# Optimization experiments

Measured on AMD Instinct MI355X. Metric: run time of the kernel, lower is better.

Reference implementation:

```python
import jax, jax.numpy as jnp
import numpy as np

B, C, H, W = 4, 256, 64, 64

def _conv1x1(x, Wt, b):
    # x: [b,c,h,w], Wt: [out,in], b: [out]
    return jnp.einsum('bchw,dc->bdhw', x, Wt) + b[None, :, None, None]

def setup_inputs() -> dict:
    key = jax.random.key(0)
    ks = jax.random.split(key, 10)
    s = 1.0 / np.sqrt(C)
    return {
        'F_c': jax.random.normal(ks[0], (B, C, H, W), jnp.float32),
        'F_s': jax.random.normal(ks[1], (B, C, H, W), jnp.float32),
        'Wf': jax.random.normal(ks[2], (C, C), jnp.float32) * s,
        'bf': jnp.zeros((C,), jnp.float32),
        'Wg': jax.random.normal(ks[3], (C, C), jnp.float32) * s,
        'bg': jnp.zeros((C,), jnp.float32),
        'Wh': jax.random.normal(ks[4], (C, C), jnp.float32) * s,
        'bh': jnp.zeros((C,), jnp.float32),
        'Wo': jax.random.normal(ks[5], (C, C), jnp.float32) * s,
        'bo': jnp.zeros((C,), jnp.float32),
    }

def reference(F_c, F_s, Wf, bf, Wg, bg, Wh, bh, Wo, bo):
    b, c, h, w = F_c.shape
    Fq = _conv1x1(F_c, Wf, bf).reshape(b, c, -1)          # [b,c,Nc]
    G = _conv1x1(F_s, Wg, bg).reshape(b, c, -1)           # [b,c,Ns]
    Hv = _conv1x1(F_s, Wh, bh).reshape(b, c, -1)          # [b,c,Ns]
    S = jnp.einsum('bcn,bcm->bnm', Fq, G)                 # [b,Nc,Ns] (unscaled)
    S = jax.nn.softmax(S, axis=-1)
    res = jnp.einsum('bcm,bnm->bcn', Hv, S)               # [b,c,Nc]
    res = res.reshape(b, c, h, w)
    return _conv1x1(res, Wo, bo)
```

## Files before the change

### kernel.cpp

```cpp
#include <hip/hip_runtime.h>
#include <stdint.h>

#define NB 4
#define CC 256
#define NN 4096
#define KITERS 32

typedef __attribute__((ext_vector_type(8))) _Float16 half8;
typedef __attribute__((ext_vector_type(4))) _Float16 half4;
typedef __attribute__((ext_vector_type(2))) _Float16 half2v;
typedef __attribute__((ext_vector_type(4))) float floatx4;
typedef __attribute__((ext_vector_type(16))) float float16v;
typedef __attribute__((ext_vector_type(4))) int intx4;

__device__ __forceinline__ void cvt16(const float4* src, half8& lo, half8& hi) {
  float4 a = src[0], b = src[1], c = src[2], d = src[3];
  lo[0] = (_Float16)a.x; lo[1] = (_Float16)a.y; lo[2] = (_Float16)a.z; lo[3] = (_Float16)a.w;
  lo[4] = (_Float16)b.x; lo[5] = (_Float16)b.y; lo[6] = (_Float16)b.z; lo[7] = (_Float16)b.w;
  hi[0] = (_Float16)c.x; hi[1] = (_Float16)c.y; hi[2] = (_Float16)c.z; hi[3] = (_Float16)c.w;
  hi[4] = (_Float16)d.x; hi[5] = (_Float16)d.y; hi[6] = (_Float16)d.z; hi[7] = (_Float16)d.w;
}

__global__ __launch_bounds__(256) void k_transpose(const float* __restrict__ Fc,
                                                   const float* __restrict__ Fs,
                                                   _Float16* __restrict__ Xct,
                                                   _Float16* __restrict__ Xst) {
  __shared__ float t[64][65];
  const int nt = blockIdx.x, ct = blockIdx.y, bz = blockIdx.z;
  const int b = bz >> 1;
  const float* src = ((bz & 1) ? Fs : Fc) + (size_t)b * CC * NN;
  _Float16* dst = ((bz & 1) ? Xst : Xct) + (size_t)b * NN * CC;
  const int tid = threadIdx.x;
  const int n0 = nt * 64, c0 = ct * 64;
  const int col = tid & 63, row4 = tid >> 6;
#pragma unroll
  for (int i = 0; i < 16; i++) {
    int c = row4 + i * 4;
    t[c][col] = src[(size_t)(c0 + c) * NN + n0 + col];
  }
  __syncthreads();
#pragma unroll
  for (int i = 0; i < 16; i++) {
    int n = row4 + i * 4;
    dst[(size_t)(n0 + n) * CC + c0 + col] = (_Float16)t[col][n];
  }
}

__global__ __launch_bounds__(256, 2) void k_qkv(const float* __restrict__ Wf,
                                                const float* __restrict__ Wg,
                                                const float* __restrict__ Wh,
                                                const _Float16* __restrict__ Xct,
                                                const _Float16* __restrict__ Xst,
                                                const float* __restrict__ bf,
                                                const float* __restrict__ bg,
                                                const float* __restrict__ bh,
                                                _Float16* __restrict__ Qf,
                                                _Float16* __restrict__ Kf,
                                                _Float16* __restrict__ Vtf) {
  __shared__ _Float16 As[128][40];
  __shared__ _Float16 Bs[128][40];
  const int z = blockIdx.z, bz = blockIdx.y;
  const float* W = (z == 0) ? Wf : ((z == 1) ? Wg : Wh);
  const _Float16* X = ((z == 0) ? Xct : Xst) + (size_t)bz * NN * CC;
  const float* bias = (z == 0) ? bf : ((z == 1) ? bg : bh);
  int mt, nt;
  if (z < 2) { mt = blockIdx.x >> 5; nt = blockIdx.x & 31; }
  else       { mt = blockIdx.x >> 1; nt = blockIdx.x & 1;  }
  const int m0 = mt * 128, n0 = nt * 128;
  const int tid = threadIdx.x;
  const int wave = tid >> 6, lane = tid & 63, quad = lane >> 4, l15 = lane & 15;
  const int wm = (wave >> 1) * 64, wn = (wave & 1) * 64;

  floatx4 acc[4][4];
#pragma unroll
  for (int i = 0; i < 4; i++)
#pragma unroll
    for (int j = 0; j < 4; j++) acc[i][j] = (floatx4){0.f, 0.f, 0.f, 0.f};

  const int srow = tid >> 1;
  const int shalf = (tid & 1) * 16;

  for (int kk = 0; kk < 256; kk += 32) {
    half8 a_lo, a_hi, b_lo, b_hi;
    if (z < 2) {
      cvt16((const float4*)(W + (size_t)(m0 + srow) * 256 + kk + shalf), a_lo, a_hi);
      const _Float16* bp = X + (size_t)(n0 + srow) * 256 + kk + shalf;
      b_lo = *(const half8*)bp; b_hi = *(const half8*)(bp + 8);
    } else {
      const _Float16* ap = X + (size_t)(m0 + srow) * 256 + kk + shalf;
      a_lo = *(const half8*)ap; a_hi = *(const half8*)(ap + 8);
      cvt16((const float4*)(W + (size_t)(n0 + srow) * 256 + kk + shalf), b_lo, b_hi);
    }
    __syncthreads();
    *(half8*)&As[srow][shalf] = a_lo;
    *(half8*)&As[srow][shalf + 8] = a_hi;
    *(half8*)&Bs[srow][shalf] = b_lo;
    *(half8*)&Bs[srow][shalf + 8] = b_hi;
    __syncthreads();
    half8 af[4], bfr[4];
#pragma unroll
    for (int mb = 0; mb < 4; mb++) af[mb] = *(const half8*)&As[wm + mb * 16 + l15][quad * 8];
#pragma unroll
    for (int nb = 0; nb < 4; nb++) bfr[nb] = *(const half8*)&Bs[wn + nb * 16 + l15][quad * 8];
#pragma unroll
    for (int mb = 0; mb < 4; mb++)
#pragma unroll
      for (int nb = 0; nb < 4; nb++)
        acc[mb][nb] = __builtin_amdgcn_mfma_f32_16x16x32_f16(af[mb], bfr[nb], acc[mb][nb], 0, 0, 0);
  }

  if (z < 2) {
    _Float16* op = (z == 0 ? Qf : Kf) + (size_t)bz * NN * CC;
#pragma unroll
    for (int mb = 0; mb < 4; mb++) {
      int d0 = m0 + wm + mb * 16 + quad * 4;
      float b0 = bias[d0], b1 = bias[d0 + 1], b2 = bias[d0 + 2], b3 = bias[d0 + 3];
#pragma unroll
      for (int nb = 0; nb < 4; nb++) {
        int n_ = n0 + wn + nb * 16 + l15;
        half4 pk;
        pk[0] = (_Float16)(acc[mb][nb][0] + b0);
        pk[1] = (_Float16)(acc[mb][nb][1] + b1);
        pk[2] = (_Float16)(acc[mb][nb][2] + b2);
        pk[3] = (_Float16)(acc[mb][nb][3] + b3);
        *(half4*)(op + (size_t)n_ * CC + d0) = pk;
      }
    }
  } else {
    _Float16* op = Vtf + (size_t)bz * NN * CC;
#pragma unroll
    for (int mb = 0; mb < 4; mb++) {
      int nq0 = m0 + wm + mb * 16 + quad * 4;
#pragma unroll
      for (int nb = 0; nb < 4; nb++) {
        int d = n0 + wn + nb * 16 + l15;
        float bv = bias[d];
        half4 pk;
        pk[0] = (_Float16)(acc[mb][nb][0] + bv);
        pk[1] = (_Float16)(acc[mb][nb][1] + bv);
        pk[2] = (_Float16)(acc[mb][nb][2] + bv);
        pk[3] = (_Float16)(acc[mb][nb][3] + bv);
        *(half4*)(op + (size_t)d * NN + nq0) = pk;
      }
    }
  }
}

__global__ __launch_bounds__(256, 2) void k_attn(const _Float16* __restrict__ Q,
                                                 const _Float16* __restrict__ K,
                                                 const _Float16* __restrict__ Vt,
                                                 _Float16* __restrict__ Opart,
                                                 float2* __restrict__ Ml) {
  __shared__ _Float16 Kl[32][264];
  __shared__ _Float16 Vl[2][256][40];
  __shared__ _Float16 Pl[4][32][40];

  const int qt = blockIdx.x, ck = blockIdx.y, b = blockIdx.z;
  const int tid = threadIdx.x;
  const int wave = tid >> 6, lane = tid & 63;
  const int ql = lane & 31, h = lane >> 5;
  const int q0 = qt * 128 + wave * 32;
  const _Float16* Qb = Q + (size_t)b * NN * CC;
  const _Float16* Kb = K + (size_t)b * NN * CC;
  const _Float16* Vb = Vt + (size_t)b * CC * NN;
  const int k_base = ck * 1024;

  half8 qf[16];
#pragma unroll
  for (int cs = 0; cs < 16; cs++)
    qf[cs] = *(const half8*)(Qb + (size_t)(q0 + ql) * CC + cs * 16 + h * 8);

  float16v Oa[8];
#pragma unroll
  for (int g = 0; g < 8; g++)
#pragma unroll
    for (int i = 0; i < 16; i++) Oa[g][i] = 0.f;

  float m_run = -1e30f, l_run = 0.f;

  const int krow = tid >> 4;
  const int kcol = (tid & 15) * 16;
  const int vrow = tid >> 2;
  const int vcol = (tid & 3) * 8;

  intx4 kpre[4], vpre[4];
  {
    const _Float16* g = Kb + (size_t)k_base * CC;
    kpre[0] = *(const intx4*)(g + (size_t)krow * CC + kcol);
    kpre[1] = *(const intx4*)(g + (size_t)krow * CC + kcol + 8);
    kpre[2] = *(const intx4*)(g + (size_t)(krow + 16) * CC + kcol);
    kpre[3] = *(const intx4*)(g + (size_t)(krow + 16) * CC + kcol + 8);
#pragma unroll
    for (int p = 0; p < 4; p++)
      vpre[p] = *(const intx4*)(Vb + (size_t)(vrow + 64 * p) * NN + k_base + vcol);
  }

  for (int t = 0; t < KITERS; t++) {
    const int vb = t & 1;
    __syncthreads();
    *(intx4*)&Kl[krow][kcol] = kpre[0];
    *(intx4*)&Kl[krow][kcol + 8] = kpre[1];
    *(intx4*)&Kl[krow + 16][kcol] = kpre[2];
    *(intx4*)&Kl[krow + 16][kcol + 8] = kpre[3];
#pragma unroll
    for (int p = 0; p < 4; p++) *(intx4*)&Vl[vb][vrow + 64 * p][vcol] = vpre[p];
    __syncthreads();
    if (t + 1 < KITERS) {
      const int k0n = k_base + (t + 1) * 32;
      const _Float16* g = Kb + (size_t)k0n * CC;
      kpre[0] = *(const intx4*)(g + (size_t)krow * CC + kcol);
      kpre[1] = *(const intx4*)(g + (size_t)krow * CC + kcol + 8);
      kpre[2] = *(const intx4*)(g + (size_t)(krow + 16) * CC + kcol);
      kpre[3] = *(const intx4*)(g + (size_t)(krow + 16) * CC + kcol + 8);
#pragma unroll
      for (int p = 0; p < 4; p++)
        vpre[p] = *(const intx4*)(Vb + (size_t)(vrow + 64 * p) * NN + k0n + vcol);
    }

    float16v s;
#pragma unroll
    for (int i = 0; i < 16; i++) s[i] = 0.f;
    if (t > 0) {
      const int vr = vb ^ 1;
      half8 pf0 = *(const half8*)&Pl[wave][ql][h * 8];
      half8 pf1 = *(const half8*)&Pl[wave][ql][16 + h * 8];
#pragma unroll
      for (int u = 0; u < 8; u++) {
        half8 kfa = *(const half8*)&Kl[ql][(2 * u) * 16 + h * 8];
        s = __builtin_amdgcn_mfma_f32_32x32x16_f16(kfa, qf[2 * u], s, 0, 0, 0);
        half8 vfa = *(const half8*)&Vl[vr][u * 32 + ql][h * 8];
        Oa[u] = __builtin_amdgcn_mfma_f32_32x32x16_f16(vfa, pf0, Oa[u], 0, 0, 0);
        half8 kfb = *(const half8*)&Kl[ql][(2 * u + 1) * 16 + h * 8];
        s = __builtin_amdgcn_mfma_f32_32x32x16_f16(kfb, qf[2 * u + 1], s, 0, 0, 0);
        half8 vfb = *(const half8*)&Vl[vr][u * 32 + ql][16 + h * 8];
        Oa[u] = __builtin_amdgcn_mfma_f32_32x32x16_f16(vfb, pf1, Oa[u], 0, 0, 0);
      }
    } else {
#pragma unroll
      for (int cs = 0; cs < 16; cs++) {
        half8 kf = *(const half8*)&Kl[ql][cs * 16 + h * 8];
        s = __builtin_amdgcn_mfma_f32_32x32x16_f16(kf, qf[cs], s, 0, 0, 0);
      }
    }

    float tmax = s[0];
#pragma unroll
    for (int i = 1; i < 16; i++) tmax = fmaxf(tmax, s[i]);
    tmax = fmaxf(tmax, __shfl_xor(tmax, 32));
    bool need = tmax > m_run + 8.0f;
    if (__any((int)need)) {
      float mN = need ? tmax : m_run;
      float alpha = __expf(m_run - mN);
      m_run = mN;
      l_run *= alpha;
#pragma unroll
      for (int g = 0; g < 8; g++)
#pragma unroll
        for (int i = 0; i < 16; i++) Oa[g][i] *= alpha;
    }
    float ts = 0.f;
#pragma unroll
    for (int i = 0; i < 16; i++) {
      float p = __expf(s[i] - m_run);
      s[i] = p;
      ts += p;
    }
    ts += __shfl_xor(ts, 32);
    l_run += ts;
#pragma unroll
    for (int r = 0; r < 16; r += 2) {
      half2v pk;
      pk[0] = (_Float16)s[r];
      pk[1] = (_Float16)s[r + 1];
      int kk2 = (r & 3) + 8 * (r >> 2) + 4 * h;
      *(half2v*)&Pl[wave][ql][kk2] = pk;
    }
  }

  {
    const int vr = (KITERS - 1) & 1;
    half8 pf0 = *(const half8*)&Pl[wave][ql][h * 8];
    half8 pf1 = *(const half8*)&Pl[wave][ql][16 + h * 8];
#pragma unroll
    for (int u = 0; u < 8; u++) {
      half8 vfa = *(const half8*)&Vl[vr][u * 32 + ql][h * 8];
      Oa[u] = __builtin_amdgcn_mfma_f32_32x32x16_f16(vfa, pf0, Oa[u], 0, 0, 0);
      half8 vfb = *(const half8*)&Vl[vr][u * 32 + ql][16 + h * 8];
      Oa[u] = __builtin_amdgcn_mfma_f32_32x32x16_f16(vfb, pf1, Oa[u], 0, 0, 0);
    }
  }

  float invl = 1.f / l_run;
  __syncthreads();
  float* ot = (float*)(&Kl[0][0]) + wave * (32 * 33);
  _Float16* Opb = Opart + ((size_t)ck * NB + b) * NN * CC;
  const int qr = lane >> 1;
  const int chalf = (lane & 1) * 16;
#pragma unroll
  for (int g = 0; g < 8; g++) {
#pragma unroll
    for (int r = 0; r < 16; r++)
      ot[((r & 3) + 8 * (r >> 2) + 4 * h) * 33 + ql] = Oa[g][r] * invl;
    __builtin_amdgcn_s_waitcnt(0);
    half8 o0, o1;
#pragma unroll
    for (int i = 0; i < 8; i++) o0[i] = (_Float16)ot[(chalf + i) * 33 + qr];
#pragma unroll
    for (int i = 0; i < 8; i++) o1[i] = (_Float16)ot[(chalf + 8 + i) * 33 + qr];
    _Float16* gp = Opb + (size_t)(q0 + qr) * CC + g * 32 + chalf;
    *(half8*)gp = o0;
    *(half8*)(gp + 8) = o1;
    __builtin_amdgcn_s_waitcnt(0);
  }
  if (h == 0) {
    float2 ml; ml.x = m_run; ml.y = l_run;
    Ml[((size_t)ck * NB + b) * NN + q0 + ql] = ml;
  }
}

__global__ __launch_bounds__(256) void k_merge(const _Float16* __restrict__ Opart,
                                               const float2* __restrict__ Ml,
                                               _Float16* __restrict__ Om) {
  const int b = blockIdx.y, t = threadIdx.x;
  const int q = blockIdx.x * 32 + (t >> 3);
  const int c0 = (t & 7) * 32;
  const size_t qi = (size_t)b * NN + q;
  float2 m0 = Ml[qi], m1 = Ml[(size_t)NB * NN + qi];
  float2 m2 = Ml[(size_t)2 * NB * NN + qi], m3 = Ml[(size_t)3 * NB * NN + qi];
  float M = fmaxf(fmaxf(m0.x, m1.x), fmaxf(m2.x, m3.x));
  float w0 = __expf(m0.x - M) * m0.y, w1 = __expf(m1.x - M) * m1.y;
  float w2 = __expf(m2.x - M) * m2.y, w3 = __expf(m3.x - M) * m3.y;
  float inv = 1.f / (w0 + w1 + w2 + w3);
  w0 *= inv; w1 *= inv; w2 *= inv; w3 *= inv;
  const size_t off = qi * CC + c0;
  const size_t ps = (size_t)NB * NN * CC;
  const _Float16* p0 = Opart + off;
  const _Float16* p1 = Opart + ps + off;
  const _Float16* p2 = Opart + 2 * ps + off;
  const _Float16* p3 = Opart + 3 * ps + off;
  _Float16* o = Om + off;
#pragma unroll
  for (int u = 0; u < 4; u++) {
    half8 a0 = *(const half8*)(p0 + u * 8);
    half8 a1 = *(const half8*)(p1 + u * 8);
    half8 a2 = *(const half8*)(p2 + u * 8);
    half8 a3 = *(const half8*)(p3 + u * 8);
    half8 r;
#pragma unroll
    for (int i = 0; i < 8; i++)
      r[i] = (_Float16)(w0 * (float)a0[i] + w1 * (float)a1[i] +
                        w2 * (float)a2[i] + w3 * (float)a3[i]);
    *(half8*)(o + u * 8) = r;
  }
}

__global__ __launch_bounds__(256, 2) void k_out(const _Float16* __restrict__ Om,
                                                const float* __restrict__ Wo,
                                                const float* __restrict__ bo,
                                                float* __restrict__ out) {
  __shared__ _Float16 As[128][40];
  __shared__ _Float16 Bs[128][40];
  const int bz = blockIdx.y;
  const int mt = blockIdx.x >> 1, nt = blockIdx.x & 1;
  const int m0 = mt * 128, n0 = nt * 128;
  const int tid = threadIdx.x;
  const int wave = tid >> 6, lane = tid & 63, quad = lane >> 4, l15 = lane & 15;
  const int wm = (wave >> 1) * 64, wn = (wave & 1) * 64;
  const _Float16* X = Om + (size_t)bz * NN * CC;

  floatx4 acc[4][4];
#pragma unroll
  for (int i = 0; i < 4; i++)
#pragma unroll
    for (int j = 0; j < 4; j++) acc[i][j] = (floatx4){0.f, 0.f, 0.f, 0.f};

  const int srow = tid >> 1;
  const int shalf = (tid & 1) * 16;

  for (int kk = 0; kk < 256; kk += 32) {
    const _Float16* ap = X + (size_t)(m0 + srow) * 256 + kk + shalf;
    half8 a_lo = *(const half8*)ap;
    half8 a_hi = *(const half8*)(ap + 8);
    half8 b_lo, b_hi;
    cvt16((const float4*)(Wo + (size_t)(n0 + srow) * 256 + kk + shalf), b_lo, b_hi);
    __syncthreads();
    *(half8*)&As[srow][shalf] = a_lo;
    *(half8*)&As[srow][shalf + 8] = a_hi;
    *(half8*)&Bs[srow][shalf] = b_lo;
    *(half8*)&Bs[srow][shalf + 8] = b_hi;
    __syncthreads();
    half8 af[4], bfr[4];
#pragma unroll
    for (int mb = 0; mb < 4; mb++) af[mb] = *(const half8*)&As[wm + mb * 16 + l15][quad * 8];
#pragma unroll
    for (int nb = 0; nb < 4; nb++) bfr[nb] = *(const half8*)&Bs[wn + nb * 16 + l15][quad * 8];
#pragma unroll
    for (int mb = 0; mb < 4; mb++)
#pragma unroll
      for (int nb = 0; nb < 4; nb++)
        acc[mb][nb] = __builtin_amdgcn_mfma_f32_16x16x32_f16(af[mb], bfr[nb], acc[mb][nb], 0, 0, 0);
  }

  float* op = out + (size_t)bz * NN * CC;
#pragma unroll
  for (int mb = 0; mb < 4; mb++) {
    int nq0 = m0 + wm + mb * 16 + quad * 4;
#pragma unroll
    for (int nb = 0; nb < 4; nb++) {
      int d = n0 + wn + nb * 16 + l15;
      float bv = bo[d];
      floatx4 pk;
      pk[0] = acc[mb][nb][0] + bv;
      pk[1] = acc[mb][nb][1] + bv;
      pk[2] = acc[mb][nb][2] + bv;
      pk[3] = acc[mb][nb][3] + bv;
      *(floatx4*)(op + (size_t)d * NN + nq0) = pk;
    }
  }
}

extern "C" void kernel_launch(void* const* d_in, const int* in_sizes, int n_in,
                              void* d_out, int out_size, void* d_ws, size_t ws_size,
                              hipStream_t stream) {
  const float* Fc = (const float*)d_in[0];
  const float* Fs = (const float*)d_in[1];
  const float* Wf = (const float*)d_in[2];
  const float* bf_ = (const float*)d_in[3];
  const float* Wg = (const float*)d_in[4];
  const float* bg = (const float*)d_in[5];
  const float* Wh = (const float*)d_in[6];
  const float* bh = (const float*)d_in[7];
  const float* Wo = (const float*)d_in[8];
  const float* bo = (const float*)d_in[9];

  char* ws = (char*)d_ws;
  const size_t sz = (size_t)NB * NN * CC * sizeof(_Float16);
  _Float16* Xct = (_Float16*)(ws + 0 * sz);
  _Float16* Xst = (_Float16*)(ws + 1 * sz);
  _Float16* Opart = Xct;
  _Float16* Qf  = (_Float16*)(ws + 4 * sz);
  _Float16* Kf  = (_Float16*)(ws + 5 * sz);
  _Float16* Vtf = (_Float16*)(ws + 6 * sz);
  _Float16* Om  = Qf;
  float2* Ml = (float2*)(ws + 7 * sz);

  k_transpose<<<dim3(64, 4, 8), 256, 0, stream>>>(Fc, Fs, Xct, Xst);
  k_qkv<<<dim3(64, NB, 3), 256, 0, stream>>>(Wf, Wg, Wh, Xct, Xst, bf_, bg, bh, Qf, Kf, Vtf);
  k_attn<<<dim3(32, 4, NB), 256, 0, stream>>>(Qf, Kf, Vtf, Opart, Ml);
  k_merge<<<dim3(128, NB), 256, 0, stream>>>(Opart, Ml, Om);
  k_out<<<dim3(64, NB), 256, 0, stream>>>(Om, Wo, bo, (float*)d_out);
}
```

Baseline: 226.9 us.

## Pre-swizzle Q/K/V into MFMA fragment order and fuse split-K merge into output GEMM

The QKV projection now writes Q, K and V directly in a tiled MFMA-fragment layout. The attention kernel can then load tiles with contiguous, conflict-free vector copies and read fragments with lane-linear LDS accesses instead of padded strided arrays. The separate merge kernel is removed: the output projection combines the four split-K partials with their softmax weights while it loads its A operand. This saves one launch and one intermediate round trip. It also narrows the epilogue waitcnt to LGKM only and uses tree reductions for the row max and sum, at the cost of scattered stores in the QKV epilogue.

```diff
diff --git a/kernel.cpp b/kernel.cpp
--- a/kernel.cpp
+++ b/kernel.cpp
@@ -5,6 +5,7 @@
 #define CC 256
 #define NN 4096
 #define KITERS 32
+#define WAIT_LGKM0 0xC07F
 
 typedef __attribute__((ext_vector_type(8))) _Float16 half8;
 typedef __attribute__((ext_vector_type(4))) _Float16 half4;
@@ -54,9 +55,9 @@
                                                 const float* __restrict__ bf,
                                                 const float* __restrict__ bg,
                                                 const float* __restrict__ bh,
-                                                _Float16* __restrict__ Qf,
-                                                _Float16* __restrict__ Kf,
-                                                _Float16* __restrict__ Vtf) {
+                                                _Float16* __restrict__ Qs,
+                                                _Float16* __restrict__ Ks,
+                                                _Float16* __restrict__ Vs) {
   __shared__ _Float16 As[128][40];
   __shared__ _Float16 Bs[128][40];
   const int z = blockIdx.z, bz = blockIdx.y;
@@ -110,37 +111,44 @@
   }
 
   if (z < 2) {
-    _Float16* op = (z == 0 ? Qf : Kf) + (size_t)bz * NN * CC;
+    _Float16* op = (z == 0 ? Qs : Ks) + (size_t)bz * NN * CC;
 #pragma unroll
     for (int mb = 0; mb < 4; mb++) {
       int d0 = m0 + wm + mb * 16 + quad * 4;
       float b0 = bias[d0], b1 = bias[d0 + 1], b2 = bias[d0 + 2], b3 = bias[d0 + 3];
+      const int cs = d0 >> 4, hh = (d0 >> 3) & 1, j0 = d0 & 7;
 #pragma unroll
       for (int nb = 0; nb < 4; nb++) {
         int n_ = n0 + wn + nb * 16 + l15;
+        int kt = n_ >> 5, ql_ = n_ & 31;
         half4 pk;
         pk[0] = (_Float16)(acc[mb][nb][0] + b0);
         pk[1] = (_Float16)(acc[mb][nb][1] + b1);
         pk[2] = (_Float16)(acc[mb][nb][2] + b2);
         pk[3] = (_Float16)(acc[mb][nb][3] + b3);
-        *(half4*)(op + (size_t)n_ * CC + d0) = pk;
+        size_t idx = ((size_t)(kt * 16 + cs) * 64 + ql_ + 32 * hh) * 8 + j0;
+        *(half4*)(op + idx) = pk;
       }
     }
   } else {
-    _Float16* op = Vtf + (size_t)bz * NN * CC;
+    _Float16* op = Vs + (size_t)bz * NN * CC;
 #pragma unroll
     for (int mb = 0; mb < 4; mb++) {
       int nq0 = m0 + wm + mb * 16 + quad * 4;
+      const int kt = nq0 >> 5, krel = nq0 & 31;
+      const int hk = krel >> 4, hh = (krel >> 3) & 1, j0 = krel & 7;
 #pragma unroll
       for (int nb = 0; nb < 4; nb++) {
         int d = n0 + wn + nb * 16 + l15;
+        int ql_ = d & 31, g = (d >> 5) & 7;
         float bv = bias[d];
         half4 pk;
         pk[0] = (_Float16)(acc[mb][nb][0] + bv);
         pk[1] = (_Float16)(acc[mb][nb][1] + bv);
         pk[2] = (_Float16)(acc[mb][nb][2] + bv);
         pk[3] = (_Float16)(acc[mb][nb][3] + bv);
-        *(half4*)(op + (size_t)d * NN + nq0) = pk;
+        size_t idx = (((size_t)(kt * 8 + g) * 2 + hk) * 64 + ql_ + 32 * hh) * 8 + j0;
+        *(half4*)(op + idx) = pk;
       }
     }
   }
@@ -151,24 +159,25 @@
                                                  const _Float16* __restrict__ Vt,
                                                  _Float16* __restrict__ Opart,
                                                  float2* __restrict__ Ml) {
-  __shared__ _Float16 Kl[32][264];
-  __shared__ _Float16 Vl[2][256][40];
-  __shared__ _Float16 Pl[4][32][40];
-
-  const int qt = blockIdx.x, ck = blockIdx.y, b = blockIdx.z;
+  __shared__ _Float16 smem[8192 * 3 + 4096];
   const int tid = threadIdx.x;
   const int wave = tid >> 6, lane = tid & 63;
+  _Float16* Kl = smem;
+  _Float16* Plw = smem + 3 * 8192 + wave * 1024;
+
+  const int qt = blockIdx.x, ck = blockIdx.y, b = blockIdx.z;
   const int ql = lane & 31, h = lane >> 5;
   const int q0 = qt * 128 + wave * 32;
   const _Float16* Qb = Q + (size_t)b * NN * CC;
   const _Float16* Kb = K + (size_t)b * NN * CC;
-  const _Float16* Vb = Vt + (size_t)b * CC * NN;
-  const int k_base = ck * 1024;
-
+  const _Float16* Vb = Vt + (size_t)b * NN * CC;
+  const int kt_base = ck * (1024 / 32);
+
+  const int ktq = q0 >> 5;
   half8 qf[16];
 #pragma unroll
   for (int cs = 0; cs < 16; cs++)
-    qf[cs] = *(const half8*)(Qb + (size_t)(q0 + ql) * CC + cs * 16 + h * 8);
+    qf[cs] = *(const half8*)(Qb + ((size_t)(ktq * 16 + cs) * 64 + lane) * 8);
 
   float16v Oa[8];
 #pragma unroll
@@ -177,75 +186,70 @@
     for (int i = 0; i < 16; i++) Oa[g][i] = 0.f;
 
   float m_run = -1e30f, l_run = 0.f;
-
-  const int krow = tid >> 4;
-  const int kcol = (tid & 15) * 16;
-  const int vrow = tid >> 2;
-  const int vcol = (tid & 3) * 8;
 
   intx4 kpre[4], vpre[4];
   {
-    const _Float16* g = Kb + (size_t)k_base * CC;
-    kpre[0] = *(const intx4*)(g + (size_t)krow * CC + kcol);
-    kpre[1] = *(const intx4*)(g + (size_t)krow * CC + kcol + 8);
-    kpre[2] = *(const intx4*)(g + (size_t)(krow + 16) * CC + kcol);
-    kpre[3] = *(const intx4*)(g + (size_t)(krow + 16) * CC + kcol + 8);
-#pragma unroll
-    for (int p = 0; p < 4; p++)
-      vpre[p] = *(const intx4*)(Vb + (size_t)(vrow + 64 * p) * NN + k_base + vcol);
+    const _Float16* Kt = Kb + (size_t)kt_base * 8192;
+    const _Float16* Vtile = Vb + (size_t)kt_base * 8192;
+#pragma unroll
+    for (int p = 0; p < 4; p++) {
+      kpre[p] = *(const intx4*)(Kt + tid * 8 + p * 2048);
+      vpre[p] = *(const intx4*)(Vtile + tid * 8 + p * 2048);
+    }
   }
 
   for (int t = 0; t < KITERS; t++) {
     const int vb = t & 1;
-    __syncthreads();
-    *(intx4*)&Kl[krow][kcol] = kpre[0];
-    *(intx4*)&Kl[krow][kcol + 8] = kpre[1];
-    *(intx4*)&Kl[krow + 16][kcol] = kpre[2];
-    *(intx4*)&Kl[krow + 16][kcol + 8] = kpre[3];
-#pragma unroll
-    for (int p = 0; p < 4; p++) *(intx4*)&Vl[vb][vrow + 64 * p][vcol] = vpre[p];
+    _Float16* Vw = smem + (1 + vb) * 8192;
+    __syncthreads();
+#pragma unroll
+    for (int p = 0; p < 4; p++) {
+      *(intx4*)(Kl + tid * 8 + p * 2048) = kpre[p];
+      *(intx4*)(Vw + tid * 8 + p * 2048) = vpre[p];
+    }
     __syncthreads();
     if (t + 1 < KITERS) {
-      const int k0n = k_base + (t + 1) * 32;
-      const _Float16* g = Kb + (size_t)k0n * CC;
-      kpre[0] = *(const intx4*)(g + (size_t)krow * CC + kcol);
-      kpre[1] = *(const intx4*)(g + (size_t)krow * CC + kcol + 8);
-      kpre[2] = *(const intx4*)(g + (size_t)(krow + 16) * CC + kcol);
-      kpre[3] = *(const intx4*)(g + (size_t)(krow + 16) * CC + kcol + 8);
-#pragma unroll
-      for (int p = 0; p < 4; p++)
-        vpre[p] = *(const intx4*)(Vb + (size_t)(vrow + 64 * p) * NN + k0n + vcol);
+      const _Float16* Kt = Kb + (size_t)(kt_base + t + 1) * 8192;
+      const _Float16* Vtile = Vb + (size_t)(kt_base + t + 1) * 8192;
+#pragma unroll
+      for (int p = 0; p < 4; p++) {
+        kpre[p] = *(const intx4*)(Kt + tid * 8 + p * 2048);
+        vpre[p] = *(const intx4*)(Vtile + tid * 8 + p * 2048);
+      }
     }
 
     float16v s;
 #pragma unroll
     for (int i = 0; i < 16; i++) s[i] = 0.f;
     if (t > 0) {
-      const int vr = vb ^ 1;
-      half8 pf0 = *(const half8*)&Pl[wave][ql][h * 8];
-      half8 pf1 = *(const half8*)&Pl[wave][ql][16 + h * 8];
+      _Float16* Vr = smem + (1 + (vb ^ 1)) * 8192;
+      half8 pf0 = *(const half8*)(Plw + lane * 8);
+      half8 pf1 = *(const half8*)(Plw + 512 + lane * 8);
 #pragma unroll
       for (int u = 0; u < 8; u++) {
-        half8 kfa = *(const half8*)&Kl[ql][(2 * u) * 16 + h * 8];
+        half8 kfa = *(const half8*)(Kl + (2 * u) * 512 + lane * 8);
         s = __builtin_amdgcn_mfma_f32_32x32x16_f16(kfa, qf[2 * u], s, 0, 0, 0);
-        half8 vfa = *(const half8*)&Vl[vr][u * 32 + ql][h * 8];
+        half8 vfa = *(const half8*)(Vr + (u * 2) * 512 + lane * 8);
         Oa[u] = __builtin_amdgcn_mfma_f32_32x32x16_f16(vfa, pf0, Oa[u], 0, 0, 0);
-        half8 kfb = *(const half8*)&Kl[ql][(2 * u + 1) * 16 + h * 8];
+        half8 kfb = *(const half8*)(Kl + (2 * u + 1) * 512 + lane * 8);
         s = __builtin_amdgcn_mfma_f32_32x32x16_f16(kfb, qf[2 * u + 1], s, 0, 0, 0);
-        half8 vfb = *(const half8*)&Vl[vr][u * 32 + ql][16 + h * 8];
+        half8 vfb = *(const half8*)(Vr + (u * 2 + 1) * 512 + lane * 8);
         Oa[u] = __builtin_amdgcn_mfma_f32_32x32x16_f16(vfb, pf1, Oa[u], 0, 0, 0);
       }
     } else {
 #pragma unroll
       for (int cs = 0; cs < 16; cs++) {
-        half8 kf = *(const half8*)&Kl[ql][cs * 16 + h * 8];
+        half8 kf = *(const half8*)(Kl + cs * 512 + lane * 8);
         s = __builtin_amdgcn_mfma_f32_32x32x16_f16(kf, qf[cs], s, 0, 0, 0);
       }
     }
 
-    float tmax = s[0];
-#pragma unroll
-    for (int i = 1; i < 16; i++) tmax = fmaxf(tmax, s[i]);
+    float t0 = fmaxf(s[0], s[1]), t1 = fmaxf(s[2], s[3]);
+    float t2 = fmaxf(s[4], s[5]), t3 = fmaxf(s[6], s[7]);
+    float t4 = fmaxf(s[8], s[9]), t5 = fmaxf(s[10], s[11]);
+    float t6 = fmaxf(s[12], s[13]), t7 = fmaxf(s[14], s[15]);
+    t0 = fmaxf(t0, t1); t2 = fmaxf(t2, t3); t4 = fmaxf(t4, t5); t6 = fmaxf(t6, t7);
+    float tmax = fmaxf(fmaxf(t0, t2), fmaxf(t4, t6));
     tmax = fmaxf(tmax, __shfl_xor(tmax, 32));
     bool need = tmax > m_run + 8.0f;
     if (__any((int)need)) {
@@ -258,13 +262,13 @@
 #pragma unroll
         for (int i = 0; i < 16; i++) Oa[g][i] *= alpha;
     }
-    float ts = 0.f;
-#pragma unroll
-    for (int i = 0; i < 16; i++) {
-      float p = __expf(s[i] - m_run);
-      s[i] = p;
-      ts += p;
-    }
+#pragma unroll
+    for (int i = 0; i < 16; i++) s[i] = __expf(s[i] - m_run);
+    float u0 = (s[0] + s[1]) + (s[2] + s[3]);
+    float u1 = (s[4] + s[5]) + (s[6] + s[7]);
+    float u2 = (s[8] + s[9]) + (s[10] + s[11]);
+    float u3 = (s[12] + s[13]) + (s[14] + s[15]);
+    float ts = (u0 + u1) + (u2 + u3);
     ts += __shfl_xor(ts, 32);
     l_run += ts;
 #pragma unroll
@@ -272,27 +276,27 @@
       half2v pk;
       pk[0] = (_Float16)s[r];
       pk[1] = (_Float16)s[r + 1];
-      int kk2 = (r & 3) + 8 * (r >> 2) + 4 * h;
-      *(half2v*)&Pl[wave][ql][kk2] = pk;
+      int k = (r & 3) + 8 * (r >> 2) + 4 * h;
+      *(half2v*)(Plw + (k >> 4) * 512 + (ql + 32 * ((k >> 3) & 1)) * 8 + (k & 7)) = pk;
     }
   }
 
   {
-    const int vr = (KITERS - 1) & 1;
-    half8 pf0 = *(const half8*)&Pl[wave][ql][h * 8];
-    half8 pf1 = *(const half8*)&Pl[wave][ql][16 + h * 8];
+    _Float16* Vr = smem + (1 + ((KITERS - 1) & 1)) * 8192;
+    half8 pf0 = *(const half8*)(Plw + lane * 8);
+    half8 pf1 = *(const half8*)(Plw + 512 + lane * 8);
 #pragma unroll
     for (int u = 0; u < 8; u++) {
-      half8 vfa = *(const half8*)&Vl[vr][u * 32 + ql][h * 8];
+      half8 vfa = *(const half8*)(Vr + (u * 2) * 512 + lane * 8);
       Oa[u] = __builtin_amdgcn_mfma_f32_32x32x16_f16(vfa, pf0, Oa[u], 0, 0, 0);
-      half8 vfb = *(const half8*)&Vl[vr][u * 32 + ql][16 + h * 8];
+      half8 vfb = *(const half8*)(Vr + (u * 2 + 1) * 512 + lane * 8);
       Oa[u] = __builtin_amdgcn_mfma_f32_32x32x16_f16(vfb, pf1, Oa[u], 0, 0, 0);
     }
   }
 
   float invl = 1.f / l_run;
   __syncthreads();
-  float* ot = (float*)(&Kl[0][0]) + wave * (32 * 33);
+  float* ot = (float*)smem + wave * (32 * 33);
   _Float16* Opb = Opart + ((size_t)ck * NB + b) * NN * CC;
   const int qr = lane >> 1;
   const int chalf = (lane & 1) * 16;
@@ -301,7 +305,7 @@
 #pragma unroll
     for (int r = 0; r < 16; r++)
       ot[((r & 3) + 8 * (r >> 2) + 4 * h) * 33 + ql] = Oa[g][r] * invl;
-    __builtin_amdgcn_s_waitcnt(0);
+    __builtin_amdgcn_s_waitcnt(WAIT_LGKM0);
     half8 o0, o1;
 #pragma unroll
     for (int i = 0; i < 8; i++) o0[i] = (_Float16)ot[(chalf + i) * 33 + qr];
@@ -310,7 +314,7 @@
     _Float16* gp = Opb + (size_t)(q0 + qr) * CC + g * 32 + chalf;
     *(half8*)gp = o0;
     *(half8*)(gp + 8) = o1;
-    __builtin_amdgcn_s_waitcnt(0);
+    __builtin_amdgcn_s_waitcnt(WAIT_LGKM0);
   }
   if (h == 0) {
     float2 ml; ml.x = m_run; ml.y = l_run;
@@ -318,43 +322,8 @@
   }
 }
 
-__global__ __launch_bounds__(256) void k_merge(const _Float16* __restrict__ Opart,
-                                               const float2* __restrict__ Ml,
-                                               _Float16* __restrict__ Om) {
-  const int b = blockIdx.y, t = threadIdx.x;
-  const int q = blockIdx.x * 32 + (t >> 3);
-  const int c0 = (t & 7) * 32;
-  const size_t qi = (size_t)b * NN + q;
-  float2 m0 = Ml[qi], m1 = Ml[(size_t)NB * NN + qi];
-  float2 m2 = Ml[(size_t)2 * NB * NN + qi], m3 = Ml[(size_t)3 * NB * NN + qi];
-  float M = fmaxf(fmaxf(m0.x, m1.x), fmaxf(m2.x, m3.x));
-  float w0 = __expf(m0.x - M) * m0.y, w1 = __expf(m1.x - M) * m1.y;
-  float w2 = __expf(m2.x - M) * m2.y, w3 = __expf(m3.x - M) * m3.y;
-  float inv = 1.f / (w0 + w1 + w2 + w3);
-  w0 *= inv; w1 *= inv; w2 *= inv; w3 *= inv;
-  const size_t off = qi * CC + c0;
-  const size_t ps = (size_t)NB * NN * CC;
-  const _Float16* p0 = Opart + off;
-  const _Float16* p1 = Opart + ps + off;
-  const _Float16* p2 = Opart + 2 * ps + off;
-  const _Float16* p3 = Opart + 3 * ps + off;
-  _Float16* o = Om + off;
-#pragma unroll
-  for (int u = 0; u < 4; u++) {
-    half8 a0 = *(const half8*)(p0 + u * 8);
-    half8 a1 = *(const half8*)(p1 + u * 8);
-    half8 a2 = *(const half8*)(p2 + u * 8);
-    half8 a3 = *(const half8*)(p3 + u * 8);
-    half8 r;
-#pragma unroll
-    for (int i = 0; i < 8; i++)
-      r[i] = (_Float16)(w0 * (float)a0[i] + w1 * (float)a1[i] +
-                        w2 * (float)a2[i] + w3 * (float)a3[i]);
-    *(half8*)(o + u * 8) = r;
-  }
-}
-
-__global__ __launch_bounds__(256, 2) void k_out(const _Float16* __restrict__ Om,
+__global__ __launch_bounds__(256, 2) void k_out(const _Float16* __restrict__ Opart,
+                                                const float2* __restrict__ Ml,
                                                 const float* __restrict__ Wo,
                                                 const float* __restrict__ bo,
                                                 float* __restrict__ out) {
@@ -366,7 +335,6 @@
   const int tid = threadIdx.x;
   const int wave = tid >> 6, lane = tid & 63, quad = lane >> 4, l15 = lane & 15;
   const int wm = (wave >> 1) * 64, wn = (wave & 1) * 64;
-  const _Float16* X = Om + (size_t)bz * NN * CC;
 
   floatx4 acc[4][4];
 #pragma unroll
@@ -377,15 +345,36 @@
   const int srow = tid >> 1;
   const int shalf = (tid & 1) * 16;
 
+  const size_t qi = (size_t)bz * NN + m0 + srow;
+  float2 a0 = Ml[qi], a1 = Ml[(size_t)NB * NN + qi];
+  float2 a2 = Ml[(size_t)2 * NB * NN + qi], a3 = Ml[(size_t)3 * NB * NN + qi];
+  float M = fmaxf(fmaxf(a0.x, a1.x), fmaxf(a2.x, a3.x));
+  float w0 = __expf(a0.x - M) * a0.y, w1 = __expf(a1.x - M) * a1.y;
+  float w2 = __expf(a2.x - M) * a2.y, w3 = __expf(a3.x - M) * a3.y;
+  float inv = 1.f / (w0 + w1 + w2 + w3);
+  w0 *= inv; w1 *= inv; w2 *= inv; w3 *= inv;
+  const size_t ps = (size_t)NB * NN * CC;
+  const _Float16* prow = Opart + qi * CC;
+
   for (int kk = 0; kk < 256; kk += 32) {
-    const _Float16* ap = X + (size_t)(m0 + srow) * 256 + kk + shalf;
-    half8 a_lo = *(const half8*)ap;
-    half8 a_hi = *(const half8*)(ap + 8);
+    const _Float16* pr = prow + kk + shalf;
+    half8 p0a = *(const half8*)pr,            p0b = *(const half8*)(pr + 8);
+    half8 p1a = *(const half8*)(pr + ps),     p1b = *(const half8*)(pr + ps + 8);
+    half8 p2a = *(const half8*)(pr + 2 * ps), p2b = *(const half8*)(pr + 2 * ps + 8);
+    half8 p3a = *(const half8*)(pr + 3 * ps), p3b = *(const half8*)(pr + 3 * ps + 8);
+    half8 ma, mb2;
+#pragma unroll
+    for (int i = 0; i < 8; i++) {
+      ma[i] = (_Float16)(w0 * (float)p0a[i] + w1 * (float)p1a[i] +
+                         w2 * (float)p2a[i] + w3 * (float)p3a[i]);
+      mb2[i] = (_Float16)(w0 * (float)p0b[i] + w1 * (float)p1b[i] +
+                          w2 * (float)p2b[i] + w3 * (float)p3b[i]);
+    }
     half8 b_lo, b_hi;
     cvt16((const float4*)(Wo + (size_t)(n0 + srow) * 256 + kk + shalf), b_lo, b_hi);
     __syncthreads();
-    *(half8*)&As[srow][shalf] = a_lo;
-    *(half8*)&As[srow][shalf + 8] = a_hi;
+    *(half8*)&As[srow][shalf] = ma;
+    *(half8*)&As[srow][shalf + 8] = mb2;
     *(half8*)&Bs[srow][shalf] = b_lo;
     *(half8*)&Bs[srow][shalf + 8] = b_hi;
     __syncthreads();
@@ -438,15 +427,13 @@
   _Float16* Xct = (_Float16*)(ws + 0 * sz);
   _Float16* Xst = (_Float16*)(ws + 1 * sz);
   _Float16* Opart = Xct;
-  _Float16* Qf  = (_Float16*)(ws + 4 * sz);
-  _Float16* Kf  = (_Float16*)(ws + 5 * sz);
-  _Float16* Vtf = (_Float16*)(ws + 6 * sz);
-  _Float16* Om  = Qf;
+  _Float16* Qs = (_Float16*)(ws + 4 * sz);
+  _Float16* Ks = (_Float16*)(ws + 5 * sz);
+  _Float16* Vs = (_Float16*)(ws + 6 * sz);
   float2* Ml = (float2*)(ws + 7 * sz);
 
   k_transpose<<<dim3(64, 4, 8), 256, 0, stream>>>(Fc, Fs, Xct, Xst);
-  k_qkv<<<dim3(64, NB, 3), 256, 0, stream>>>(Wf, Wg, Wh, Xct, Xst, bf_, bg, bh, Qf, Kf, Vtf);
-  k_attn<<<dim3(32, 4, NB), 256, 0, stream>>>(Qf, Kf, Vtf, Opart, Ml);
-  k_merge<<<dim3(128, NB), 256, 0, stream>>>(Opart, Ml, Om);
-  k_out<<<dim3(64, NB), 256, 0, stream>>>(Om, Wo, bo, (float*)d_out);
-}
+  k_qkv<<<dim3(64, NB, 3), 256, 0, stream>>>(Wf, Wg, Wh, Xct, Xst, bf_, bg, bh, Qs, Ks, Vs);
+  k_attn<<<dim3(32, 4, NB), 256, 0, stream>>>(Qs, Ks, Vs, Opart, Ml);
+  k_out<<<dim3(64, NB), 256, 0, stream>>>(Opart, Ml, Wo, bo, (float*)d_out);
+}
```

New measurement: 216.5 us. 4.6% less time.
